# Optimization experiments

Hardware: AMD Instinct MI355X
Metric: run time of the kernel (lower is better)

The kernel has to match this reference:

```python
import jax, jax.numpy as jnp
import numpy as np

B, L, V, E, H = 64, 512, 256, 512, 1024


def setup_inputs() -> dict:
    key = jax.random.key(0)
    ks = jax.random.split(key, 6)
    s = lambda n: 1.0 / np.sqrt(n)
    return {
        "x": jax.random.randint(ks[0], (B, L), 0, V),
        "emb": jax.random.normal(ks[1], (V, E), jnp.float32),
        "U_w": jax.random.normal(ks[2], (H, E), jnp.float32) * s(E),
        "V_w": jax.random.normal(ks[3], (H, H), jnp.float32) * s(H),
        "alpha": jnp.ones((H,), jnp.float32),
        "beta1": jnp.ones((H,), jnp.float32),
        "beta2": jnp.ones((H,), jnp.float32),
        "bias": jnp.zeros((H,), jnp.float32),
        "dec_w": jax.random.normal(ks[4], (V, H), jnp.float32) * s(H),
        "dec_b": jnp.zeros((V,), jnp.float32),
    }


def reference(x, emb, U_w, V_w, alpha, beta1, beta2, bias, dec_w, dec_b):
    e = emb[x]                                   # [B, L, E]
    # Precompute input projection for all timesteps (U has no bias)
    Ux = jnp.einsum("ble,he->blh", e, U_w)       # [B, L, H]
    h0 = jnp.zeros((x.shape[0], V_w.shape[0]), e.dtype)

    def step(h, ux_t):
        Vh = h @ V_w.T                           # [B, H]
        m = alpha * (Vh * ux_t) + beta1 * Vh + beta2 * ux_t + bias
        h_new = jnp.tanh(m)
        return h_new, h_new

    h_last, hs = jax.lax.scan(step, h0, jnp.swapaxes(Ux, 0, 1))  # hs: [L, B, H]
    out = jnp.swapaxes(hs, 0, 1)                 # [B, L, H]
    logits = jnp.einsum("blh,vh->blv", out, dec_w) + dec_b
    return logits, h_last[None, :, :]
```

## Files before the change

### kernel.cpp

```cpp
#include <hip/hip_runtime.h>

#define DI __device__ __forceinline__

typedef short s16x4 __attribute__((ext_vector_type(4)));
typedef short s16x8 __attribute__((ext_vector_type(8)));
typedef float f32x4 __attribute__((ext_vector_type(4)));

constexpr int CB = 64, CL = 512, CV = 256, CE = 512, CH = 1024;
constexpr int CBL = CB * CL;
constexpr size_t LOGN = (size_t)CBL * CV;
constexpr unsigned SLOT = (unsigned)CB * CH * 2;

constexpr size_t WS_BAR   = 0;
constexpr size_t WS_RING  = 4096;
constexpr size_t WS_EMBB  = WS_RING + 2u*SLOT;
constexpr size_t WS_UWB   = WS_EMBB + (size_t)CV*CE*2;
constexpr size_t WS_VWB   = WS_UWB  + (size_t)CH*CE*2;
constexpr size_t WS_DECWB = WS_VWB  + (size_t)CH*CH*2;
constexpr size_t WS_UX    = WS_DECWB+ (size_t)CV*CH*2;
constexpr size_t WS_HS    = WS_UX   + (size_t)CBL*CH*2;

DI unsigned short f2bf(float f) {
  unsigned u = __float_as_uint(f);
  u += 0x7FFFu + ((u >> 16) & 1u);
  return (unsigned short)(u >> 16);
}
DI float bf2f(unsigned short h) { return __uint_as_float(((unsigned)h) << 16); }

DI f32x4 mfma_bf16(s16x8 a, s16x8 b, f32x4 c) {
  return __builtin_amdgcn_mfma_f32_16x16x32_bf16(a, b, c, 0, 0, 0);
}

DI float fast_tanh(float x) {
  float a = fminf(fabsf(x), 20.0f);
  float e = __expf(-2.0f * a);
  float r = (1.0f - e) / (1.0f + e);
  return __builtin_copysignf(r, x);
}

__global__ __launch_bounds__(256) void k_convert(
    const float* __restrict__ emb, const float* __restrict__ uw,
    const float* __restrict__ vw,  const float* __restrict__ dw,
    unsigned short* __restrict__ embb, unsigned short* __restrict__ uwb,
    unsigned short* __restrict__ vwb,  unsigned short* __restrict__ dwb)
{
  int i = (blockIdx.x * 256 + threadIdx.x) * 4;
  const float* s; unsigned short* d; int off;
  if      (i < 131072)  { s = emb; d = embb; off = i; }
  else if (i < 655360)  { s = uw;  d = uwb;  off = i - 131072; }
  else if (i < 1703936) { s = vw;  d = vwb;  off = i - 655360; }
  else                  { s = dw;  d = dwb;  off = i - 1703936; }
  float4 v = *(const float4*)(s + off);
  ushort4 o; o.x = f2bf(v.x); o.y = f2bf(v.y); o.z = f2bf(v.z); o.w = f2bf(v.w);
  *(ushort4*)(d + off) = o;
}

template<int KD, int NT, bool GATHER, bool OUTF32>
__global__ __launch_bounds__(256) void k_gemm(
    const unsigned short* __restrict__ Asrc,
    const int* __restrict__ xidx,
    const unsigned short* __restrict__ Bsrc,
    const float* __restrict__ biasv,
    unsigned short* __restrict__ Cb,
    float* __restrict__ Cf)
{
  __shared__ unsigned char As[64 * 128];
  __shared__ unsigned char Bs[64 * 128];
  __shared__ int xs[64];

  const int tid = threadIdx.x;
  const int rt = blockIdx.x, ct = blockIdx.y;
  const int r0 = rt * 64, c0 = ct * 64;

  if (GATHER) {
    if (tid < 64) xs[tid] = xidx[r0 + tid];
    __syncthreads();
  }

  const int r  = tid >> 2, kq = tid & 3;
  const unsigned short* aRow = GATHER ? (Asrc + (size_t)xs[r] * KD)
                                      : (Asrc + (size_t)(r0 + r) * KD);
  const unsigned short* bRow = Bsrc + (size_t)(c0 + r) * KD;
  const int dstOff = r * 128 + ((kq * 16) ^ ((r & 7) << 4));

  const int wave = tid >> 6, lane = tid & 63;
  const int ln15 = lane & 15, lg = lane >> 4;
  const int xr = (lane & 7) << 4;
  int aOff[4];
#pragma unroll
  for (int m = 0; m < 4; ++m) aOff[m] = (m * 16 + ln15) * 128 + ((lg * 16) ^ xr);
  const int bOff = (wave * 16 + ln15) * 128 + ((lg * 16) ^ xr);

  f32x4 acc[4] = {};
  for (int kk = 0; kk < KD / 32; ++kk) {
    s16x8 av = *(const s16x8*)(aRow + kk * 32 + kq * 8);
    s16x8 bv = *(const s16x8*)(bRow + kk * 32 + kq * 8);
    __syncthreads();
    *(s16x8*)(As + dstOff) = av;
    *(s16x8*)(Bs + dstOff) = bv;
    __syncthreads();
    s16x8 bf = *(const s16x8*)(Bs + bOff);
#pragma unroll
    for (int m = 0; m < 4; ++m) {
      s16x8 af = *(const s16x8*)(As + aOff[m]);
      acc[m] = mfma_bf16(af, bf, acc[m]);
    }
  }

  const int colg = c0 + wave * 16 + ln15;
  float bv = 0.f;
  if (OUTF32) bv = biasv[colg];
#pragma unroll
  for (int m = 0; m < 4; ++m) {
#pragma unroll
    for (int rr = 0; rr < 4; ++rr) {
      int rowg = r0 + m * 16 + lg * 4 + rr;
      if (OUTF32) Cf[(size_t)rowg * NT + colg] = acc[m][rr] + bv;
      else        Cb[(size_t)rowg * NT + colg] = f2bf(acc[m][rr]);
    }
  }
}

__global__ __launch_bounds__(256, 1) void k_rec(
    const unsigned short* __restrict__ vwb,
    const unsigned short* __restrict__ ux,
    unsigned short* __restrict__ ring,
    unsigned short* __restrict__ hs,
    const float* __restrict__ alpha, const float* __restrict__ beta1,
    const float* __restrict__ beta2, const float* __restrict__ bias,
    float* __restrict__ out, int* flags)
{
  __shared__ __align__(16) unsigned char hlds[2][16 * 2048];

  const int w = blockIdx.x;
  const int bg = w >> 4, cs = w & 15;
  const int tid = threadIdx.x;
  const int wave = tid >> 6, lane = tid & 63;
  const int ln15 = lane & 15, lg = lane >> 4;
  const int b0 = bg * 16;
  const int colbase = cs * 64 + wave * 16 + lg * 4;
  const int myb = b0 + ln15;

  s16x8 breg[32];
  {
    const unsigned short* vrow = vwb + (size_t)(cs * 64 + wave * 16 + ln15) * CH + lg * 8;
#pragma unroll
    for (int kc = 0; kc < 32; ++kc) breg[kc] = *(const s16x8*)(vrow + kc * 32);
  }
#pragma unroll
  for (int kc = 0; kc < 32; ++kc) asm volatile("" : "+v"(breg[kc]));

  const float4 alv = *(const float4*)(alpha + colbase);
  const float4 b1v = *(const float4*)(beta1 + colbase);
  const float4 b2v = *(const float4*)(beta2 + colbase);
  const float4 biv = *(const float4*)(bias  + colbase);

  __amdgpu_buffer_rsrc_t rsrd = __builtin_amdgcn_make_buffer_rsrc(
      (void*)ring, (short)0, (int)(2u * SLOT), 0x00020000);

  int* gflags = flags + bg * 64;
  const int myflag = cs * 4 + wave;

  int sRow[8], sCol[8];
#pragma unroll
  for (int i = 0; i < 8; ++i) {
    const int L = i * 4096 + tid * 16;
    sRow[i] = L >> 11;
    sCol[i] = (L & 2047) ^ ((sRow[i] & 7) << 4);
  }
  const unsigned stgBase = (unsigned)(b0 * 2048);

  const int fBase = ln15 * 2048;
  const int fXor  = (ln15 & 7) << 4;

  const unsigned cellOff = (unsigned)(myb * 2048 + colbase * 2);

  s16x4 uxv = *(const s16x4*)(ux + ((size_t)myb * CL + 0) * CH + colbase);

  for (int t = 0; t < CL; ++t) {
    f32x4 vh = {};
    if (t > 0) {
      bool ok;
      do {
        int fv = __hip_atomic_load(&gflags[lane], __ATOMIC_RELAXED,
                                   __HIP_MEMORY_SCOPE_SYSTEM);
        ok = __all(fv >= t) != 0;
      } while (!ok);
      asm volatile("" ::: "memory");

      const unsigned roff = ((unsigned)((t - 1) & 1)) * SLOT + stgBase;
      s16x8 stg[8];
#pragma unroll
      for (int i = 0; i < 8; ++i) {
        auto raw = __builtin_amdgcn_raw_buffer_load_b128(
            rsrd, (int)(roff + i * 4096 + tid * 16), 0, 17);
        stg[i] = __builtin_bit_cast(s16x8, raw);
      }
      unsigned char* lb = hlds[t & 1];
#pragma unroll
      for (int i = 0; i < 8; ++i)
        *(s16x8*)(lb + sRow[i] * 2048 + sCol[i]) = stg[i];
      __syncthreads();

      f32x4 a0 = {}, a1 = {}, a2 = {}, a3 = {};
#pragma unroll
      for (int kc = 0; kc < 32; kc += 4) {
        s16x8 f0 = *(const s16x8*)(lb + fBase + ((lg * 16 + kc * 64)       ^ fXor));
        s16x8 f1 = *(const s16x8*)(lb + fBase + ((lg * 16 + kc * 64 + 64)  ^ fXor));
        s16x8 f2 = *(const s16x8*)(lb + fBase + ((lg * 16 + kc * 64 + 128) ^ fXor));
        s16x8 f3 = *(const s16x8*)(lb + fBase + ((lg * 16 + kc * 64 + 192) ^ fXor));
        a0 = mfma_bf16(breg[kc],     f0, a0);
        a1 = mfma_bf16(breg[kc + 1], f1, a1);
        a2 = mfma_bf16(breg[kc + 2], f2, a2);
        a3 = mfma_bf16(breg[kc + 3], f3, a3);
      }
      vh = (a0 + a1) + (a2 + a3);
    }

    float hnv[4]; unsigned short hbv[4];
#pragma unroll
    for (int rr = 0; rr < 4; ++rr) {
      const float u = bf2f((unsigned short)uxv[rr]);
      const float v = vh[rr];
      const float mm = (&alv.x)[rr] * (v * u) + (&b1v.x)[rr] * v +
                       (&b2v.x)[rr] * u + (&biv.x)[rr];
      hnv[rr] = fast_tanh(mm);
      hbv[rr] = f2bf(hnv[rr]);
    }

    const unsigned long long pk = (unsigned long long)hbv[0]
                                | ((unsigned long long)hbv[1] << 16)
                                | ((unsigned long long)hbv[2] << 32)
                                | ((unsigned long long)hbv[3] << 48);

    if (t < CL - 1) {
      unsigned long long* hp = (unsigned long long*)
          ((char*)ring + (size_t)(t & 1) * SLOT + cellOff);
      __hip_atomic_store(hp, pk, __ATOMIC_RELAXED, __HIP_MEMORY_SCOPE_SYSTEM);
      asm volatile("s_waitcnt vmcnt(0)" ::: "memory");
      if (lane == 0)
        __hip_atomic_store(&gflags[myflag], t + 1, __ATOMIC_RELAXED,
                           __HIP_MEMORY_SCOPE_SYSTEM);
      *(unsigned long long*)(hs + ((size_t)myb * CL + t) * CH + colbase) = pk;
      uxv = *(const s16x4*)(ux + ((size_t)myb * CL + (t + 1)) * CH + colbase);
    } else {
      *(unsigned long long*)(hs + ((size_t)myb * CL + t) * CH + colbase) = pk;
      float4 o; o.x = hnv[0]; o.y = hnv[1]; o.z = hnv[2]; o.w = hnv[3];
      *(float4*)(out + LOGN + (size_t)myb * CH + colbase) = o;
    }
  }
}

extern "C" void kernel_launch(void* const* d_in, const int* in_sizes, int n_in,
                              void* d_out, int out_size, void* d_ws, size_t ws_size,
                              hipStream_t stream) {
  const int*   x     = (const int*)  d_in[0];
  const float* emb   = (const float*)d_in[1];
  const float* Uw    = (const float*)d_in[2];
  const float* Vw    = (const float*)d_in[3];
  const float* alpha = (const float*)d_in[4];
  const float* beta1 = (const float*)d_in[5];
  const float* beta2 = (const float*)d_in[6];
  const float* bias  = (const float*)d_in[7];
  const float* decw  = (const float*)d_in[8];
  const float* decb  = (const float*)d_in[9];
  float* out = (float*)d_out;
  char*  ws  = (char*)d_ws;

  int*            flags = (int*)(ws + WS_BAR);
  unsigned short* ring  = (unsigned short*)(ws + WS_RING);
  unsigned short* embb  = (unsigned short*)(ws + WS_EMBB);
  unsigned short* uwb   = (unsigned short*)(ws + WS_UWB);
  unsigned short* vwb   = (unsigned short*)(ws + WS_VWB);
  unsigned short* dwb   = (unsigned short*)(ws + WS_DECWB);
  unsigned short* uxb   = (unsigned short*)(ws + WS_UX);
  unsigned short* hsb   = (unsigned short*)(ws + WS_HS);

  (void)hipMemsetAsync(ws + WS_BAR, 0, 4096, stream);

  k_convert<<<1920, 256, 0, stream>>>(emb, Uw, Vw, decw, embb, uwb, vwb, dwb);

  k_gemm<CE, CH, true, false><<<dim3(CBL / 64, CH / 64), 256, 0, stream>>>(
      embb, x, uwb, nullptr, uxb, nullptr);

  k_rec<<<64, 256, 0, stream>>>(vwb, uxb, ring, hsb, alpha, beta1, beta2, bias, out, flags);

  k_gemm<CH, CV, false, true><<<dim3(CBL / 64, CV / 64), 256, 0, stream>>>(
      hsb, nullptr, dwb, decb, nullptr, out);
}
```

Before: 1.631 ms.

## Co-locate recurrence batch groups on one XCD and use agent-scope sync

The recurrence kernel now launches 128 blocks and keeps only those with bid&7 < 4. Under round-robin XCD dispatch, each batch group's 16 column-slice blocks should then land on the same XCD. Each block reads its XCC_ID and publishes it to a table; if all 16 blocks in a group agree, the group uses agent-scope atomics and buffer loads with cache bits 1 instead of system-scope/coherent loads, cutting the cost of the per-step cross-block handoff. It falls back to the old system-scope path if placement differs, and it relies on the mod-8 XCD dispatch assumption and an extra startup spin.

Result: faster. 1.479 ms (-9.3%).

```diff
diff --git a/kernel.cpp b/kernel.cpp
--- a/kernel.cpp
+++ b/kernel.cpp
@@ -12,6 +12,7 @@
 constexpr unsigned SLOT = (unsigned)CB * CH * 2;
 
 constexpr size_t WS_BAR   = 0;
+constexpr size_t WS_XCDT  = 1024;
 constexpr size_t WS_RING  = 4096;
 constexpr size_t WS_EMBB  = WS_RING + 2u*SLOT;
 constexpr size_t WS_UWB   = WS_EMBB + (size_t)CV*CE*2;
@@ -121,6 +122,9 @@
   }
 }
 
+struct FastTag { static constexpr bool fast = true;  };
+struct SafeTag { static constexpr bool fast = false; };
+
 __global__ __launch_bounds__(256, 1) void k_rec(
     const unsigned short* __restrict__ vwb,
     const unsigned short* __restrict__ ux,
@@ -128,12 +132,14 @@
     unsigned short* __restrict__ hs,
     const float* __restrict__ alpha, const float* __restrict__ beta1,
     const float* __restrict__ beta2, const float* __restrict__ bias,
-    float* __restrict__ out, int* flags)
+    float* __restrict__ out, int* flags, int* xcdtab)
 {
   __shared__ __align__(16) unsigned char hlds[2][16 * 2048];
-
-  const int w = blockIdx.x;
-  const int bg = w >> 4, cs = w & 15;
+  __shared__ int smode;
+
+  const int bid = blockIdx.x;
+  const int bg = bid & 7, cs = bid >> 3;
+  if (bg >= 4) return;
   const int tid = threadIdx.x;
   const int wave = tid >> 6, lane = tid & 63;
   const int ln15 = lane & 15, lg = lane >> 4;
@@ -141,6 +147,24 @@
   const int colbase = cs * 64 + wave * 16 + lg * 4;
   const int myb = b0 + ln15;
 
+  int* gxt = xcdtab + bg * 16;
+  if (tid == 0) {
+    unsigned myxcd;
+    asm volatile("s_getreg_b32 %0, hwreg(HW_REG_XCC_ID)" : "=s"(myxcd));
+    myxcd &= 15u;
+    __hip_atomic_store(&gxt[cs], (int)myxcd, __ATOMIC_RELAXED, __HIP_MEMORY_SCOPE_SYSTEM);
+    int first = -1; bool same = true;
+    for (int i = 0; i < 16;) {
+      int v = __hip_atomic_load(&gxt[i], __ATOMIC_RELAXED, __HIP_MEMORY_SCOPE_SYSTEM);
+      if (v == -1) { __builtin_amdgcn_s_sleep(8); continue; }
+      if (first == -1) first = v; else if (v != first) same = false;
+      ++i;
+    }
+    smode = same ? 1 : 0;
+  }
+  __syncthreads();
+  const bool fastmode = (smode != 0);
+
   s16x8 breg[32];
   {
     const unsigned short* vrow = vwb + (size_t)(cs * 64 + wave * 16 + ln15) * CH + lg * 8;
@@ -172,83 +196,86 @@
 
   const int fBase = ln15 * 2048;
   const int fXor  = (ln15 & 7) << 4;
-
   const unsigned cellOff = (unsigned)(myb * 2048 + colbase * 2);
 
   s16x4 uxv = *(const s16x4*)(ux + ((size_t)myb * CL + 0) * CH + colbase);
 
-  for (int t = 0; t < CL; ++t) {
-    f32x4 vh = {};
-    if (t > 0) {
-      bool ok;
-      do {
-        int fv = __hip_atomic_load(&gflags[lane], __ATOMIC_RELAXED,
-                                   __HIP_MEMORY_SCOPE_SYSTEM);
-        ok = __all(fv >= t) != 0;
-      } while (!ok);
-      asm volatile("" ::: "memory");
-
-      const unsigned roff = ((unsigned)((t - 1) & 1)) * SLOT + stgBase;
-      s16x8 stg[8];
-#pragma unroll
-      for (int i = 0; i < 8; ++i) {
-        auto raw = __builtin_amdgcn_raw_buffer_load_b128(
-            rsrd, (int)(roff + i * 4096 + tid * 16), 0, 17);
-        stg[i] = __builtin_bit_cast(s16x8, raw);
+  auto run = [&](auto tag) {
+    constexpr int  AUX = decltype(tag)::fast ? 1 : 17;
+    constexpr auto SCP = decltype(tag)::fast ? __HIP_MEMORY_SCOPE_AGENT
+                                             : __HIP_MEMORY_SCOPE_SYSTEM;
+    for (int t = 0; t < CL; ++t) {
+      f32x4 vh = {};
+      if (t > 0) {
+        bool ok;
+        do {
+          int fv = __hip_atomic_load(&gflags[lane], __ATOMIC_RELAXED, SCP);
+          ok = __all(fv >= t) != 0;
+        } while (!ok);
+        asm volatile("" ::: "memory");
+
+        const unsigned roff = ((unsigned)((t - 1) & 1)) * SLOT + stgBase;
+        s16x8 stg[8];
+#pragma unroll
+        for (int i = 0; i < 8; ++i) {
+          auto raw = __builtin_amdgcn_raw_buffer_load_b128(
+              rsrd, (int)(roff + i * 4096 + tid * 16), 0, AUX);
+          stg[i] = __builtin_bit_cast(s16x8, raw);
+        }
+        unsigned char* lb = hlds[t & 1];
+#pragma unroll
+        for (int i = 0; i < 8; ++i)
+          *(s16x8*)(lb + sRow[i] * 2048 + sCol[i]) = stg[i];
+        __syncthreads();
+
+        f32x4 a0 = {}, a1 = {}, a2 = {}, a3 = {};
+#pragma unroll
+        for (int kc = 0; kc < 32; kc += 4) {
+          s16x8 f0 = *(const s16x8*)(lb + fBase + ((lg * 16 + kc * 64)       ^ fXor));
+          s16x8 f1 = *(const s16x8*)(lb + fBase + ((lg * 16 + kc * 64 + 64)  ^ fXor));
+          s16x8 f2 = *(const s16x8*)(lb + fBase + ((lg * 16 + kc * 64 + 128) ^ fXor));
+          s16x8 f3 = *(const s16x8*)(lb + fBase + ((lg * 16 + kc * 64 + 192) ^ fXor));
+          a0 = mfma_bf16(breg[kc],     f0, a0);
+          a1 = mfma_bf16(breg[kc + 1], f1, a1);
+          a2 = mfma_bf16(breg[kc + 2], f2, a2);
+          a3 = mfma_bf16(breg[kc + 3], f3, a3);
+        }
+        vh = (a0 + a1) + (a2 + a3);
       }
-      unsigned char* lb = hlds[t & 1];
-#pragma unroll
-      for (int i = 0; i < 8; ++i)
-        *(s16x8*)(lb + sRow[i] * 2048 + sCol[i]) = stg[i];
-      __syncthreads();
-
-      f32x4 a0 = {}, a1 = {}, a2 = {}, a3 = {};
-#pragma unroll
-      for (int kc = 0; kc < 32; kc += 4) {
-        s16x8 f0 = *(const s16x8*)(lb + fBase + ((lg * 16 + kc * 64)       ^ fXor));
-        s16x8 f1 = *(const s16x8*)(lb + fBase + ((lg * 16 + kc * 64 + 64)  ^ fXor));
-        s16x8 f2 = *(const s16x8*)(lb + fBase + ((lg * 16 + kc * 64 + 128) ^ fXor));
-        s16x8 f3 = *(const s16x8*)(lb + fBase + ((lg * 16 + kc * 64 + 192) ^ fXor));
-        a0 = mfma_bf16(breg[kc],     f0, a0);
-        a1 = mfma_bf16(breg[kc + 1], f1, a1);
-        a2 = mfma_bf16(breg[kc + 2], f2, a2);
-        a3 = mfma_bf16(breg[kc + 3], f3, a3);
+
+      float hnv[4]; unsigned short hbv[4];
+#pragma unroll
+      for (int rr = 0; rr < 4; ++rr) {
+        const float u = bf2f((unsigned short)uxv[rr]);
+        const float v = vh[rr];
+        const float mm = (&alv.x)[rr] * (v * u) + (&b1v.x)[rr] * v +
+                         (&b2v.x)[rr] * u + (&biv.x)[rr];
+        hnv[rr] = fast_tanh(mm);
+        hbv[rr] = f2bf(hnv[rr]);
       }
-      vh = (a0 + a1) + (a2 + a3);
+
+      const unsigned long long pk = (unsigned long long)hbv[0]
+                                  | ((unsigned long long)hbv[1] << 16)
+                                  | ((unsigned long long)hbv[2] << 32)
+                                  | ((unsigned long long)hbv[3] << 48);
+
+      if (t < CL - 1) {
+        unsigned long long* hp = (unsigned long long*)
+            ((char*)ring + (size_t)(t & 1) * SLOT + cellOff);
+        __hip_atomic_store(hp, pk, __ATOMIC_RELAXED, SCP);
+        asm volatile("s_waitcnt vmcnt(0)" ::: "memory");
+        if (lane == 0)
+          __hip_atomic_store(&gflags[myflag], t + 1, __ATOMIC_RELAXED, SCP);
+        *(unsigned long long*)(hs + ((size_t)myb * CL + t) * CH + colbase) = pk;
+        uxv = *(const s16x4*)(ux + ((size_t)myb * CL + (t + 1)) * CH + colbase);
+      } else {
+        *(unsigned long long*)(hs + ((size_t)myb * CL + t) * CH + colbase) = pk;
+        float4 o; o.x = hnv[0]; o.y = hnv[1]; o.z = hnv[2]; o.w = hnv[3];
+        *(float4*)(out + LOGN + (size_t)myb * CH + colbase) = o;
+      }
     }
-
-    float hnv[4]; unsigned short hbv[4];
-#pragma unroll
-    for (int rr = 0; rr < 4; ++rr) {
-      const float u = bf2f((unsigned short)uxv[rr]);
-      const float v = vh[rr];
-      const float mm = (&alv.x)[rr] * (v * u) + (&b1v.x)[rr] * v +
-                       (&b2v.x)[rr] * u + (&biv.x)[rr];
-      hnv[rr] = fast_tanh(mm);
-      hbv[rr] = f2bf(hnv[rr]);
-    }
-
-    const unsigned long long pk = (unsigned long long)hbv[0]
-                                | ((unsigned long long)hbv[1] << 16)
-                                | ((unsigned long long)hbv[2] << 32)
-                                | ((unsigned long long)hbv[3] << 48);
-
-    if (t < CL - 1) {
-      unsigned long long* hp = (unsigned long long*)
-          ((char*)ring + (size_t)(t & 1) * SLOT + cellOff);
-      __hip_atomic_store(hp, pk, __ATOMIC_RELAXED, __HIP_MEMORY_SCOPE_SYSTEM);
-      asm volatile("s_waitcnt vmcnt(0)" ::: "memory");
-      if (lane == 0)
-        __hip_atomic_store(&gflags[myflag], t + 1, __ATOMIC_RELAXED,
-                           __HIP_MEMORY_SCOPE_SYSTEM);
-      *(unsigned long long*)(hs + ((size_t)myb * CL + t) * CH + colbase) = pk;
-      uxv = *(const s16x4*)(ux + ((size_t)myb * CL + (t + 1)) * CH + colbase);
-    } else {
-      *(unsigned long long*)(hs + ((size_t)myb * CL + t) * CH + colbase) = pk;
-      float4 o; o.x = hnv[0]; o.y = hnv[1]; o.z = hnv[2]; o.w = hnv[3];
-      *(float4*)(out + LOGN + (size_t)myb * CH + colbase) = o;
-    }
-  }
+  };
+  if (fastmode) run(FastTag{}); else run(SafeTag{});
 }
 
 extern "C" void kernel_launch(void* const* d_in, const int* in_sizes, int n_in,
@@ -268,6 +295,7 @@
   char*  ws  = (char*)d_ws;
 
   int*            flags = (int*)(ws + WS_BAR);
+  int*            xcdt  = (int*)(ws + WS_XCDT);
   unsigned short* ring  = (unsigned short*)(ws + WS_RING);
   unsigned short* embb  = (unsigned short*)(ws + WS_EMBB);
   unsigned short* uwb   = (unsigned short*)(ws + WS_UWB);
@@ -276,14 +304,16 @@
   unsigned short* uxb   = (unsigned short*)(ws + WS_UX);
   unsigned short* hsb   = (unsigned short*)(ws + WS_HS);
 
-  (void)hipMemsetAsync(ws + WS_BAR, 0, 4096, stream);
+  (void)hipMemsetAsync(ws + WS_BAR, 0, 1024, stream);
+  (void)hipMemsetAsync(ws + WS_XCDT, 0xFF, 256, stream);
 
   k_convert<<<1920, 256, 0, stream>>>(emb, Uw, Vw, decw, embb, uwb, vwb, dwb);
 
   k_gemm<CE, CH, true, false><<<dim3(CBL / 64, CH / 64), 256, 0, stream>>>(
       embb, x, uwb, nullptr, uxb, nullptr);
 
-  k_rec<<<64, 256, 0, stream>>>(vwb, uxb, ring, hsb, alpha, beta1, beta2, bias, out, flags);
+  k_rec<<<128, 256, 0, stream>>>(vwb, uxb, ring, hsb, alpha, beta1, beta2, bias,
+                                 out, flags, xcdt);
 
   k_gemm<CH, CV, false, true><<<dim3(CBL / 64, CV / 64), 256, 0, stream>>>(
       hsb, nullptr, dwb, decb, nullptr, out);
```

## Pair two batch groups per block and overlap their recurrence steps

Applied to the files above, without the earlier changes.

The recurrence kernel drops from 64 blocks of 256 threads to 32 blocks of 512 threads. Each block handles one column slice for two batch groups, with four waves per group and separate LDS buffers. Staging loads for both groups are issued right after the flag polls, so one group's MFMA and pointwise work can overlap the other's global-to-LDS transfer, and the Ux inputs are prefetched two steps ahead. The cost is that two groups now share one block's barriers, so a slow group can stall the other. Each block also does a second poll and a second __syncthreads per step.

New measurement: 5.460 ms. 3.35x slower.

```diff
diff --git a/kernel.cpp b/kernel.cpp
--- a/kernel.cpp
+++ b/kernel.cpp
@@ -121,7 +121,7 @@
   }
 }
 
-__global__ __launch_bounds__(256, 1) void k_rec(
+__global__ __launch_bounds__(512, 1) void k_rec(
     const unsigned short* __restrict__ vwb,
     const unsigned short* __restrict__ ux,
     unsigned short* __restrict__ ring,
@@ -130,20 +130,24 @@
     const float* __restrict__ beta2, const float* __restrict__ bias,
     float* __restrict__ out, int* flags)
 {
-  __shared__ __align__(16) unsigned char hlds[2][16 * 2048];
-
-  const int w = blockIdx.x;
-  const int bg = w >> 4, cs = w & 15;
+  __shared__ __align__(16) unsigned char ldsA[16 * 2048];
+  __shared__ __align__(16) unsigned char ldsB[16 * 2048];
+
+  const int bid = blockIdx.x;
+  const int cs = bid >> 1, pair = bid & 1;
+  const int bgA = pair * 2, bgB = pair * 2 + 1;
   const int tid = threadIdx.x;
   const int wave = tid >> 6, lane = tid & 63;
   const int ln15 = lane & 15, lg = lane >> 4;
-  const int b0 = bg * 16;
-  const int colbase = cs * 64 + wave * 16 + lg * 4;
-  const int myb = b0 + ln15;
+  const bool isA = (wave < 4);
+  const int w4 = wave & 3;
+  const int mybg = isA ? bgA : bgB;
+  const int myb = mybg * 16 + ln15;
+  const int colbase = cs * 64 + w4 * 16 + lg * 4;
 
   s16x8 breg[32];
   {
-    const unsigned short* vrow = vwb + (size_t)(cs * 64 + wave * 16 + ln15) * CH + lg * 8;
+    const unsigned short* vrow = vwb + (size_t)(cs * 64 + w4 * 16 + ln15) * CH + lg * 8;
 #pragma unroll
     for (int kc = 0; kc < 32; ++kc) breg[kc] = *(const s16x8*)(vrow + kc * 32);
   }
@@ -158,66 +162,61 @@
   __amdgpu_buffer_rsrc_t rsrd = __builtin_amdgcn_make_buffer_rsrc(
       (void*)ring, (short)0, (int)(2u * SLOT), 0x00020000);
 
-  int* gflags = flags + bg * 64;
-  const int myflag = cs * 4 + wave;
-
-  int sRow[8], sCol[8];
-#pragma unroll
-  for (int i = 0; i < 8; ++i) {
-    const int L = i * 4096 + tid * 16;
+  int* pfA = flags + bgA * 64;
+  int* pfB = flags + bgB * 64;
+  int* myf = flags + mybg * 64 + (cs * 4 + w4);
+
+  int sRow[4], sCol[4];
+#pragma unroll
+  for (int i = 0; i < 4; ++i) {
+    const int L = i * 8192 + tid * 16;
     sRow[i] = L >> 11;
-    sCol[i] = (L & 2047) ^ ((sRow[i] & 7) << 4);
-  }
-  const unsigned stgBase = (unsigned)(b0 * 2048);
+    sCol[i] = (L & 2047) ^ ((sRow[i] & 15) << 4);
+  }
+  const unsigned baseA = (unsigned)(bgA * 16 * 2048);
+  const unsigned baseB = (unsigned)(bgB * 16 * 2048);
 
   const int fBase = ln15 * 2048;
-  const int fXor  = (ln15 & 7) << 4;
-
+  const int fXor  = ln15 << 4;
   const unsigned cellOff = (unsigned)(myb * 2048 + colbase * 2);
 
-  s16x4 uxv = *(const s16x4*)(ux + ((size_t)myb * CL + 0) * CH + colbase);
-
-  for (int t = 0; t < CL; ++t) {
-    f32x4 vh = {};
-    if (t > 0) {
-      bool ok;
-      do {
-        int fv = __hip_atomic_load(&gflags[lane], __ATOMIC_RELAXED,
-                                   __HIP_MEMORY_SCOPE_SYSTEM);
-        ok = __all(fv >= t) != 0;
-      } while (!ok);
-      asm volatile("" ::: "memory");
-
-      const unsigned roff = ((unsigned)((t - 1) & 1)) * SLOT + stgBase;
-      s16x8 stg[8];
-#pragma unroll
-      for (int i = 0; i < 8; ++i) {
-        auto raw = __builtin_amdgcn_raw_buffer_load_b128(
-            rsrd, (int)(roff + i * 4096 + tid * 16), 0, 17);
-        stg[i] = __builtin_bit_cast(s16x8, raw);
-      }
-      unsigned char* lb = hlds[t & 1];
-#pragma unroll
-      for (int i = 0; i < 8; ++i)
-        *(s16x8*)(lb + sRow[i] * 2048 + sCol[i]) = stg[i];
-      __syncthreads();
-
-      f32x4 a0 = {}, a1 = {}, a2 = {}, a3 = {};
-#pragma unroll
-      for (int kc = 0; kc < 32; kc += 4) {
-        s16x8 f0 = *(const s16x8*)(lb + fBase + ((lg * 16 + kc * 64)       ^ fXor));
-        s16x8 f1 = *(const s16x8*)(lb + fBase + ((lg * 16 + kc * 64 + 64)  ^ fXor));
-        s16x8 f2 = *(const s16x8*)(lb + fBase + ((lg * 16 + kc * 64 + 128) ^ fXor));
-        s16x8 f3 = *(const s16x8*)(lb + fBase + ((lg * 16 + kc * 64 + 192) ^ fXor));
-        a0 = mfma_bf16(breg[kc],     f0, a0);
-        a1 = mfma_bf16(breg[kc + 1], f1, a1);
-        a2 = mfma_bf16(breg[kc + 2], f2, a2);
-        a3 = mfma_bf16(breg[kc + 3], f3, a3);
-      }
-      vh = (a0 + a1) + (a2 + a3);
-    }
-
-    float hnv[4]; unsigned short hbv[4];
+  auto pollwait = [&](int* pf, int target) {
+    bool ok;
+    do {
+      int v = __hip_atomic_load(&pf[lane], __ATOMIC_RELAXED, __HIP_MEMORY_SCOPE_SYSTEM);
+      ok = __all(v >= target) != 0;
+    } while (!ok);
+    asm volatile("" ::: "memory");
+  };
+  auto issue_stg = [&](s16x8* dst, unsigned roff) {
+#pragma unroll
+    for (int i = 0; i < 4; ++i) {
+      auto raw = __builtin_amdgcn_raw_buffer_load_b128(
+          rsrd, (int)(roff + i * 8192 + tid * 16), 0, 17);
+      dst[i] = __builtin_bit_cast(s16x8, raw);
+    }
+  };
+  auto lds_write = [&](unsigned char* lb, const s16x8* src) {
+#pragma unroll
+    for (int i = 0; i < 4; ++i)
+      *(s16x8*)(lb + sRow[i] * 2048 + sCol[i]) = src[i];
+  };
+  auto do_mfma = [&](const unsigned char* lb) {
+    f32x4 a0 = {}, a1 = {}, a2 = {}, a3 = {};
+#pragma unroll
+    for (int kc = 0; kc < 32; kc += 4) {
+      s16x8 f0 = *(const s16x8*)(lb + fBase + ((lg * 16 + kc * 64)       ^ fXor));
+      s16x8 f1 = *(const s16x8*)(lb + fBase + ((lg * 16 + kc * 64 + 64)  ^ fXor));
+      s16x8 f2 = *(const s16x8*)(lb + fBase + ((lg * 16 + kc * 64 + 128) ^ fXor));
+      s16x8 f3 = *(const s16x8*)(lb + fBase + ((lg * 16 + kc * 64 + 192) ^ fXor));
+      a0 = mfma_bf16(breg[kc],     f0, a0);
+      a1 = mfma_bf16(breg[kc + 1], f1, a1);
+      a2 = mfma_bf16(breg[kc + 2], f2, a2);
+      a3 = mfma_bf16(breg[kc + 3], f3, a3);
+    }
+    return (a0 + a1) + (a2 + a3);
+  };
+  auto pointwise = [&](f32x4 vh, const s16x4& uxv, float* hnv, unsigned short* hbv) {
 #pragma unroll
     for (int rr = 0; rr < 4; ++rr) {
       const float u = bf2f((unsigned short)uxv[rr]);
@@ -227,26 +226,88 @@
       hnv[rr] = fast_tanh(mm);
       hbv[rr] = f2bf(hnv[rr]);
     }
-
+  };
+  auto uxaddr = [&](int t) { return (const s16x4*)(ux + ((size_t)myb * CL + t) * CH + colbase); };
+
+  s16x4 ux_c = *uxaddr(0), ux_1 = *uxaddr(1), ux_2 = *uxaddr(2);
+
+  s16x8 stgA[4], stgB[4];
+
+  {
+    float hnv[4]; unsigned short hbv[4];
+    pointwise(f32x4{}, ux_c, hnv, hbv);
     const unsigned long long pk = (unsigned long long)hbv[0]
                                 | ((unsigned long long)hbv[1] << 16)
                                 | ((unsigned long long)hbv[2] << 32)
                                 | ((unsigned long long)hbv[3] << 48);
+    __hip_atomic_store((unsigned long long*)((char*)ring + cellOff), pk,
+                       __ATOMIC_RELAXED, __HIP_MEMORY_SCOPE_SYSTEM);
+    asm volatile("s_waitcnt vmcnt(0)" ::: "memory");
+    if (lane == 0)
+      __hip_atomic_store(myf, 1, __ATOMIC_RELAXED, __HIP_MEMORY_SCOPE_SYSTEM);
+    *(unsigned long long*)(hs + ((size_t)myb * CL + 0) * CH + colbase) = pk;
+    pollwait(pfA, 1); issue_stg(stgA, baseA);
+    pollwait(pfB, 1); issue_stg(stgB, baseB);
+  }
+
+  for (int t = 1; t < CL; ++t) {
+    ux_c = ux_1; ux_1 = ux_2;
+    if (t + 2 < CL) ux_2 = *uxaddr(t + 2);
+
+    lds_write(ldsA, stgA);
+    __syncthreads();
+    if (isA) {
+      f32x4 vh = do_mfma(ldsA);
+      float hnv[4]; unsigned short hbv[4];
+      pointwise(vh, ux_c, hnv, hbv);
+      const unsigned long long pk = (unsigned long long)hbv[0]
+                                  | ((unsigned long long)hbv[1] << 16)
+                                  | ((unsigned long long)hbv[2] << 32)
+                                  | ((unsigned long long)hbv[3] << 48);
+      if (t < CL - 1) {
+        __hip_atomic_store((unsigned long long*)
+            ((char*)ring + (size_t)(t & 1) * SLOT + cellOff), pk,
+            __ATOMIC_RELAXED, __HIP_MEMORY_SCOPE_SYSTEM);
+        asm volatile("s_waitcnt vmcnt(0)" ::: "memory");
+        if (lane == 0)
+          __hip_atomic_store(myf, t + 1, __ATOMIC_RELAXED, __HIP_MEMORY_SCOPE_SYSTEM);
+        *(unsigned long long*)(hs + ((size_t)myb * CL + t) * CH + colbase) = pk;
+      } else {
+        *(unsigned long long*)(hs + ((size_t)myb * CL + t) * CH + colbase) = pk;
+        float4 o; o.x = hnv[0]; o.y = hnv[1]; o.z = hnv[2]; o.w = hnv[3];
+        *(float4*)(out + LOGN + (size_t)myb * CH + colbase) = o;
+      }
+    }
+
+    lds_write(ldsB, stgB);
+    __syncthreads();
+    if (!isA) {
+      f32x4 vh = do_mfma(ldsB);
+      float hnv[4]; unsigned short hbv[4];
+      pointwise(vh, ux_c, hnv, hbv);
+      const unsigned long long pk = (unsigned long long)hbv[0]
+                                  | ((unsigned long long)hbv[1] << 16)
+                                  | ((unsigned long long)hbv[2] << 32)
+                                  | ((unsigned long long)hbv[3] << 48);
+      if (t < CL - 1) {
+        __hip_atomic_store((unsigned long long*)
+            ((char*)ring + (size_t)(t & 1) * SLOT + cellOff), pk,
+            __ATOMIC_RELAXED, __HIP_MEMORY_SCOPE_SYSTEM);
+        asm volatile("s_waitcnt vmcnt(0)" ::: "memory");
+        if (lane == 0)
+          __hip_atomic_store(myf, t + 1, __ATOMIC_RELAXED, __HIP_MEMORY_SCOPE_SYSTEM);
+        *(unsigned long long*)(hs + ((size_t)myb * CL + t) * CH + colbase) = pk;
+      } else {
+        *(unsigned long long*)(hs + ((size_t)myb * CL + t) * CH + colbase) = pk;
+        float4 o; o.x = hnv[0]; o.y = hnv[1]; o.z = hnv[2]; o.w = hnv[3];
+        *(float4*)(out + LOGN + (size_t)myb * CH + colbase) = o;
+      }
+    }
 
     if (t < CL - 1) {
-      unsigned long long* hp = (unsigned long long*)
-          ((char*)ring + (size_t)(t & 1) * SLOT + cellOff);
-      __hip_atomic_store(hp, pk, __ATOMIC_RELAXED, __HIP_MEMORY_SCOPE_SYSTEM);
-      asm volatile("s_waitcnt vmcnt(0)" ::: "memory");
-      if (lane == 0)
-        __hip_atomic_store(&gflags[myflag], t + 1, __ATOMIC_RELAXED,
-                           __HIP_MEMORY_SCOPE_SYSTEM);
-      *(unsigned long long*)(hs + ((size_t)myb * CL + t) * CH + colbase) = pk;
-      uxv = *(const s16x4*)(ux + ((size_t)myb * CL + (t + 1)) * CH + colbase);
-    } else {
-      *(unsigned long long*)(hs + ((size_t)myb * CL + t) * CH + colbase) = pk;
-      float4 o; o.x = hnv[0]; o.y = hnv[1]; o.z = hnv[2]; o.w = hnv[3];
-      *(float4*)(out + LOGN + (size_t)myb * CH + colbase) = o;
+      const unsigned so = (unsigned)(t & 1) * SLOT;
+      pollwait(pfA, t + 1); issue_stg(stgA, so + baseA);
+      pollwait(pfB, t + 1); issue_stg(stgB, so + baseB);
     }
   }
 }
@@ -276,14 +337,15 @@
   unsigned short* uxb   = (unsigned short*)(ws + WS_UX);
   unsigned short* hsb   = (unsigned short*)(ws + WS_HS);
 
-  (void)hipMemsetAsync(ws + WS_BAR, 0, 4096, stream);
+  (void)hipMemsetAsync(ws + WS_BAR, 0, 1024, stream);
 
   k_convert<<<1920, 256, 0, stream>>>(emb, Uw, Vw, decw, embb, uwb, vwb, dwb);
 
   k_gemm<CE, CH, true, false><<<dim3(CBL / 64, CH / 64), 256, 0, stream>>>(
       embb, x, uwb, nullptr, uxb, nullptr);
 
-  k_rec<<<64, 256, 0, stream>>>(vwb, uxb, ring, hsb, alpha, beta1, beta2, bias, out, flags);
+  k_rec<<<32, 512, 0, stream>>>(vwb, uxb, ring, hsb, alpha, beta1, beta2, bias,
+                                out, flags);
 
   k_gemm<CH, CV, false, true><<<dim3(CBL / 64, CV / 64), 256, 0, stream>>>(
       hsb, nullptr, dwb, decb, nullptr, out);
```
